# Kernel optimization log

Measured on AMD Instinct MI355X. Metric: run time of the kernel, lower is better.

The kernel has to match this reference:

```python
import jax, jax.numpy as jnp
import numpy as np

TGT_LEN, BS, SRC_LEN, VOCAB, DIM, EMB = 24, 16, 400, 32000, 256, 256


def setup_inputs() -> dict:
    key = jax.random.key(0)
    ks = jax.random.split(key, 16)
    g = lambda k, s, sc: jax.random.normal(k, s, dtype=jnp.float32) * sc
    return {
        "inputs": jax.random.randint(ks[0], (TGT_LEN, BS), 0, VOCAB),
        "src": jax.random.randint(ks[1], (SRC_LEN, BS), 0, VOCAB),
        "h_e": g(ks[2], (SRC_LEN, BS, DIM), 0.1),
        "h0": g(ks[3], (BS, DIM), 0.1),
        "c0": g(ks[4], (BS, DIM), 0.1),
        "W_emb": g(ks[5], (VOCAB, EMB), 0.05),
        "W_ih": g(ks[6], (4 * DIM, EMB), 0.05),
        "b_ih": g(ks[7], (4 * DIM,), 0.05),
        "W_hh": g(ks[8], (4 * DIM, DIM), 0.05),
        "b_hh": g(ks[9], (4 * DIM,), 0.05),
        "W_attn_enc": g(ks[10], (DIM, DIM), 0.05),
        "W_attn_dec": g(ks[11], (DIM, DIM), 0.05),
        "W_proj": g(ks[12], (EMB, 3 * DIM), 0.05),
        "W_u": g(ks[13], (1, 3 * DIM), 0.05),
        "b_u": g(ks[14], (1,), 0.05),
        "b_out": g(ks[15], (VOCAB, 1), 0.05),
        "pad_id": 1,
    }


def reference(inputs, src, h_e, h0, c0, W_emb, W_ih, b_ih, W_hh, b_hh,
              W_attn_enc, W_attn_dec, W_proj, W_u, b_u, b_out, pad_id):
    tgt_len, bs = inputs.shape
    vocab = W_emb.shape[0]
    dim = h0.shape[1]

    emb_seq = W_emb[inputs]                       # [T, bs, emb]
    # weight-shared output projection (sect 2.4), loop-invariant -> hoisted
    W_out = jnp.tanh(W_emb @ W_proj)              # [vocab, 3*dim]
    b_out_v = b_out[:, 0]                         # [vocab]
    w_u = W_u[0]                                  # [3*dim]
    src_ids = src.T                               # [bs, src_len]
    rows = jnp.arange(bs)[:, None]
    pos = jnp.arange(tgt_len)

    def lstm_cell(x, h, c):
        gates = x @ W_ih.T + b_ih + h @ W_hh.T + b_hh
        i, f, g_, o = jnp.split(gates, 4, axis=1)
        c_new = jax.nn.sigmoid(f) * c + jax.nn.sigmoid(i) * jnp.tanh(g_)
        h_new = jax.nn.sigmoid(o) * jnp.tanh(c_new)
        return h_new, c_new

    def step(carry, xs):
        h, c, E_hist, hd_hist = carry
        emb_t, t = xs
        h, c = lstm_cell(emb_t, h, c)
        hd_t = h                                   # [bs, dim]
        # --- temporal encoder intra-attention (eq. 3-5) ---
        q = hd_t @ W_attn_enc                      # [bs, dim]
        expE = jnp.exp(jnp.einsum('bd,sbd->bs', q, h_e))  # [bs, src]
        EE = jnp.where(t == 0, expE, expE / E_hist)
        E_hist = jnp.where(t == 0, expE, E_hist + expE)
        A_e = EE / EE.sum(axis=1, keepdims=True)
        c_e = jnp.einsum('bs,sbd->bd', A_e, h_e)
        # --- decoder intra-attention over hd_history (includes current step) ---
        hd_hist = hd_hist.at[t].set(hd_t)          # [T, bs, dim]
        qd = hd_t @ W_attn_dec
        Ed = jnp.einsum('bd,tbd->bt', qd, hd_hist)
        mask = pos[None, :] <= t
        EEd = jnp.where(mask, jnp.exp(Ed), 0.0)
        A_d = EEd / EEd.sum(axis=1, keepdims=True)
        cd = jnp.einsum('bt,tbd->bd', A_d, hd_hist)
        cd_t = jnp.where(t == 0, jnp.zeros_like(cd), cd)  # t==0: cd is zeros
        # --- pointer-generator (sect 2.3) ---
        feat = jnp.concatenate([hd_t, c_e, cd_t], axis=1)   # [bs, 3*dim]
        p_switch = jax.nn.sigmoid(feat @ w_u + b_u[0])       # [bs]
        logits = feat @ W_out.T + b_out_v                     # [bs, vocab]
        logits = logits.at[:, pad_id].set(-jnp.inf)
        p_gen = jax.nn.softmax(logits, axis=1)
        copy = jnp.zeros((bs, vocab), logits.dtype).at[rows, src_ids].add(A_e)
        scores_t = (copy + p_gen) * p_switch[:, None]
        return (h, c, E_hist, hd_hist), scores_t

    hd_hist0 = jnp.zeros((tgt_len, bs, dim), h0.dtype)
    E_hist0 = jnp.ones((bs, h_e.shape[0]), h0.dtype)
    _, scores = jax.lax.scan(step, (h0, c0, E_hist0, hd_hist0), (emb_seq, pos))
    return scores  # [T, bs, vocab] mixed copy/gen distribution per step
```

## Files before the change

kernel.cpp:

```cpp
#include <hip/hip_runtime.h>
#include <cstdint>
#include <cstddef>

#define TGT   24
#define BS    16
#define SRC   400
#define VOCABN 32000
#define DIM   256
#define NROW  (TGT*BS)
#define LSTM_NBLK 4

typedef __bf16 bf16_t;
typedef __bf16 v8bf __attribute__((ext_vector_type(8)));
typedef float  v4f  __attribute__((ext_vector_type(4)));
typedef unsigned int u32;
typedef unsigned short u16;

__device__ __forceinline__ float fast_tanh(float x) {
    float e = __expf(2.f*x);
    return 1.f - 2.f/(e + 1.f);
}

__global__ void k_prep(const float* __restrict__ Whh, const float* __restrict__ Wad,
                       const float* __restrict__ he,  const float* __restrict__ Wemb,
                       const float* __restrict__ Wproj, const float* __restrict__ Wae,
                       const float* __restrict__ Wih, const int* __restrict__ inputs,
                       const float* __restrict__ h0,
                       bf16_t* o_whh, bf16_t* o_wadT, bf16_t* o_he, bf16_t* o_heT,
                       bf16_t* o_wae, bf16_t* o_wih, bf16_t* o_wprojT, bf16_t* o_embA,
                       u32* o_hpk, u32* o_zero)
{
    const long S0=262144, S1=65536, S2=1638400, S3=1638400, S4=65536, S5=262144, S6=196608, S7=98304, S8=4096, S9=768;
    const long total = S0+S1+S2+S3+S4+S5+S6+S7+S8+S9;
    for (long i = (long)blockIdx.x*blockDim.x + threadIdx.x; i < total;
         i += (long)gridDim.x*blockDim.x) {
        long j = i;
        if (j < S0) { o_whh[j] = (bf16_t)Whh[j]; continue; }           j -= S0;
        if (j < S1) { long n = j>>8, k = j&255; o_wadT[j] = (bf16_t)Wad[k*DIM + n]; continue; } j -= S1;
        if (j < S2) { o_he[j] = (bf16_t)he[j]; continue; }             j -= S2;
        if (j < S3) {
            long b = j / 102400, rem = j % 102400, d = rem / 400, s = rem % 400;
            o_heT[j] = (bf16_t)he[(s*BS + b)*DIM + d]; continue; }     j -= S3;
        if (j < S4) { o_wae[j] = (bf16_t)Wae[j]; continue; }           j -= S4;
        if (j < S5) { o_wih[j] = (bf16_t)Wih[j]; continue; }           j -= S5;
        if (j < S6) { long n = j>>8, k = j&255; o_wprojT[j] = (bf16_t)Wproj[k*768 + n]; continue; } j -= S6;
        if (j < S7) { long r = j>>8, k = j&255; o_embA[j] = (bf16_t)Wemb[(long)inputs[r]*DIM + k]; continue; } j -= S7;
        if (j < S8) {
            float v = h0[j];
            bf16_t hi = (bf16_t)v;
            bf16_t lo = (bf16_t)(v - (float)hi);
            o_hpk[j] = (u32)(*(const u16*)&hi) | ((u32)(*(const u16*)&lo) << 16);
            continue; }                                                j -= S8;
        o_zero[j] = 0;
    }
}

__device__ __forceinline__ void gemm_tile(
    const int tid, bf16_t* As, bf16_t* Bs,
    const bf16_t* __restrict__ A, const float* __restrict__ A32,
    const bf16_t* __restrict__ B,
    const int tileIdx, const int N, const int K, const int Ntiles, const int mode,
    float* __restrict__ outF, bf16_t* __restrict__ outB,
    const float* __restrict__ bias0, const float* __restrict__ bias1)
{
    const int mt   = tileIdx / Ntiles, nt = tileIdx % Ntiles;
    const int m0   = mt*128, n0 = nt*128;
    const int lane = tid & 63, wave = tid >> 6;
    const int wm   = wave >> 1, wn = wave & 1;
    const int quad = lane >> 4, l16 = lane & 15;

    v4f acc[4][4];
#pragma unroll
    for (int i=0;i<4;i++)
#pragma unroll
        for (int j=0;j<4;j++) acc[i][j] = (v4f){0.f,0.f,0.f,0.f};

    const int srow = tid >> 1, shalf = tid & 1;
    const bf16_t* Ag   = A   ? A   + (size_t)(m0+srow)*K + shalf*16 : nullptr;
    const float*  Ag32 = A32 ? A32 + (size_t)(m0+srow)*K + shalf*16 : nullptr;
    const bf16_t* Bg = B + (size_t)(n0+srow)*K + shalf*16;
    bf16_t* AsW = &As[srow*40 + shalf*16];
    bf16_t* BsW = &Bs[srow*40 + shalf*16];

    for (int kc = 0; kc < K; kc += 32) {
        __syncthreads();
        uint4 b0 = *(const uint4*)(Bg + kc);
        uint4 b1 = *(const uint4*)(Bg + kc + 8);
        if (A32) {
            float4 f0 = *(const float4*)(Ag32 + kc);
            float4 f1 = *(const float4*)(Ag32 + kc + 4);
            float4 f2 = *(const float4*)(Ag32 + kc + 8);
            float4 f3 = *(const float4*)(Ag32 + kc + 12);
            v8bf u0, u1;
            u0[0]=(bf16_t)f0.x; u0[1]=(bf16_t)f0.y; u0[2]=(bf16_t)f0.z; u0[3]=(bf16_t)f0.w;
            u0[4]=(bf16_t)f1.x; u0[5]=(bf16_t)f1.y; u0[6]=(bf16_t)f1.z; u0[7]=(bf16_t)f1.w;
            u1[0]=(bf16_t)f2.x; u1[1]=(bf16_t)f2.y; u1[2]=(bf16_t)f2.z; u1[3]=(bf16_t)f2.w;
            u1[4]=(bf16_t)f3.x; u1[5]=(bf16_t)f3.y; u1[6]=(bf16_t)f3.z; u1[7]=(bf16_t)f3.w;
            *(v8bf*)AsW = u0; *(v8bf*)(AsW+8) = u1;
        } else {
            uint4 a0 = *(const uint4*)(Ag + kc);
            uint4 a1 = *(const uint4*)(Ag + kc + 8);
            *(uint4*)AsW = a0; *(uint4*)(AsW+8) = a1;
        }
        *(uint4*)BsW = b0; *(uint4*)(BsW+8) = b1;
        __syncthreads();
        v8bf af[4], bb[4];
#pragma unroll
        for (int i=0;i<4;i++) {
            af[i] = *(const v8bf*)&As[(wm*64 + i*16 + l16)*40 + quad*8];
            bb[i] = *(const v8bf*)&Bs[(wn*64 + i*16 + l16)*40 + quad*8];
        }
#pragma unroll
        for (int i=0;i<4;i++)
#pragma unroll
            for (int j=0;j<4;j++)
                acc[i][j] = __builtin_amdgcn_mfma_f32_16x16x32_bf16(af[i], bb[j], acc[i][j], 0,0,0);
    }

#pragma unroll
    for (int i=0;i<4;i++) {
#pragma unroll
        for (int j=0;j<4;j++) {
#pragma unroll
            for (int r=0;r<4;r++) {
                const int gr = m0 + wm*64 + i*16 + quad*4 + r;
                const int gc = n0 + wn*64 + j*16 + l16;
                const float v = acc[i][j][r];
                if (mode == 0)      outF[(size_t)gr*N + gc] = v + bias0[gc] + bias1[gc];
                else if (mode == 1) outB[(size_t)gr*N + gc] = (bf16_t)fast_tanh(v);
                else if (mode == 2) outB[(size_t)gr*N + gc] = (bf16_t)v;
                else if (mode == 4) outF[(size_t)gr*N + (gc & 255)*4 + (gc >> 8)] = v + bias0[gc] + bias1[gc];
            }
        }
    }
}

__global__ __launch_bounds__(256) void k_gemm2(
    const bf16_t* __restrict__ embA, const bf16_t* __restrict__ wih,
    float* __restrict__ xg, const float* __restrict__ b_ih, const float* __restrict__ b_hh,
    const bf16_t* __restrict__ heA, const bf16_t* __restrict__ waeB, bf16_t* __restrict__ keB)
{
    __shared__ bf16_t As[128*40];
    __shared__ bf16_t Bs[128*40];
    if (blockIdx.x < 24)
        gemm_tile(threadIdx.x, As, Bs, embA, nullptr, wih, blockIdx.x, 1024, 256, 8, 4,
                  xg, nullptr, b_ih, b_hh);
    else
        gemm_tile(threadIdx.x, As, Bs, heA, nullptr, waeB, blockIdx.x - 24, 256, 256, 2, 2,
                  nullptr, keB, nullptr, nullptr);
}

__global__ __launch_bounds__(256) void k_gemm3(
    const bf16_t* __restrict__ A, const bf16_t* __restrict__ B,
    float* __restrict__ outF, const float* __restrict__ bias0,
    const int* __restrict__ padp, float* __restrict__ rsum)
{
    __shared__ bf16_t As[128*72];
    __shared__ bf16_t Bs[128*72];
    const int tid = threadIdx.x;
    const int mt = blockIdx.x / 250, nt = blockIdx.x % 250;
    const int m0 = mt*128, n0 = nt*128;
    const int lane = tid & 63, wave = tid >> 6;
    const int wm = wave >> 1, wn = wave & 1;
    const int quad = lane >> 4, l16 = lane & 15;

    v4f acc[4][4];
#pragma unroll
    for (int i=0;i<4;i++)
#pragma unroll
        for (int j=0;j<4;j++) acc[i][j] = (v4f){0.f,0.f,0.f,0.f};

    const int srow = tid >> 1, shalf = tid & 1;
    const bf16_t* Ag = A + (size_t)(m0+srow)*768 + shalf*32;
    const bf16_t* Bg = B + (size_t)(n0+srow)*768 + shalf*32;
    bf16_t* AsW = &As[srow*72 + shalf*32];
    bf16_t* BsW = &Bs[srow*72 + shalf*32];

    for (int kc = 0; kc < 768; kc += 64) {
        __syncthreads();
        uint4 a0 = *(const uint4*)(Ag + kc);
        uint4 a1 = *(const uint4*)(Ag + kc + 8);
        uint4 a2 = *(const uint4*)(Ag + kc + 16);
        uint4 a3 = *(const uint4*)(Ag + kc + 24);
        uint4 b0 = *(const uint4*)(Bg + kc);
        uint4 b1 = *(const uint4*)(Bg + kc + 8);
        uint4 b2 = *(const uint4*)(Bg + kc + 16);
        uint4 b3 = *(const uint4*)(Bg + kc + 24);
        *(uint4*)(AsW)    = a0; *(uint4*)(AsW+8)  = a1;
        *(uint4*)(AsW+16) = a2; *(uint4*)(AsW+24) = a3;
        *(uint4*)(BsW)    = b0; *(uint4*)(BsW+8)  = b1;
        *(uint4*)(BsW+16) = b2; *(uint4*)(BsW+24) = b3;
        __syncthreads();
#pragma unroll
        for (int kk = 0; kk < 2; ++kk) {
            v8bf af[4], bb[4];
#pragma unroll
            for (int i=0;i<4;i++) {
                af[i] = *(const v8bf*)&As[(wm*64 + i*16 + l16)*72 + kk*32 + quad*8];
                bb[i] = *(const v8bf*)&Bs[(wn*64 + i*16 + l16)*72 + kk*32 + quad*8];
            }
#pragma unroll
            for (int i=0;i<4;i++)
#pragma unroll
                for (int j=0;j<4;j++)
                    acc[i][j] = __builtin_amdgcn_mfma_f32_16x16x32_bf16(af[i], bb[j], acc[i][j], 0,0,0);
        }
    }

    const int pad = *padp;
    float* rs = (float*)As;
    __syncthreads();
    if (tid < 128) rs[tid] = 0.f;
    __syncthreads();
#pragma unroll
    for (int i=0;i<4;i++) {
        float rloc[4] = {0.f,0.f,0.f,0.f};
#pragma unroll
        for (int j=0;j<4;j++) {
#pragma unroll
            for (int r=0;r<4;r++) {
                const int gr = m0 + wm*64 + i*16 + quad*4 + r;
                const int gc = n0 + wn*64 + j*16 + l16;
                const float ex = (gc == pad) ? 0.f : __expf(acc[i][j][r] + bias0[gc]);
                outF[(size_t)gr*VOCABN + gc] = ex;
                rloc[r] += ex;
            }
        }
#pragma unroll
        for (int r=0;r<4;r++)
            atomicAdd(&rs[wm*64 + i*16 + quad*4 + r], rloc[r]);
    }
    __syncthreads();
    if (tid < 128) atomicAdd(&rsum[m0 + tid], rs[tid]);
}

__device__ __forceinline__ void gridbar(int* bar, int target) {
    __syncthreads();
    if (threadIdx.x == 0) {
        __threadfence();
        __hip_atomic_fetch_add(bar, 1, __ATOMIC_ACQ_REL, __HIP_MEMORY_SCOPE_AGENT);
        while (__hip_atomic_load(bar, __ATOMIC_ACQUIRE, __HIP_MEMORY_SCOPE_AGENT) < target) { }
        __threadfence();
    }
    __syncthreads();
}

__global__ __launch_bounds__(512, 2) void k_lstm(
    const bf16_t* __restrict__ Whh, const float* __restrict__ xgT,
    const float* __restrict__ c0,
    u32* __restrict__ hpk,
    float* __restrict__ hallF,
    int* __restrict__ bar)
{
    __shared__ float gl[16][260];

    const int tid = threadIdx.x;
    const int k = blockIdx.x;
    const int w = tid >> 6, lane = tid & 63;
    const int l16 = lane & 15, quad = lane >> 4;

    v8bf wb[2][8];
#pragma unroll
    for (int ct = 0; ct < 2; ++ct) {
        const int c = w*32 + ct*16 + l16;
        const int row = (c >> 6)*256 + k*64 + (c & 63);
#pragma unroll
        for (int kc = 0; kc < 8; ++kc)
            wb[ct][kc] = *(const v8bf*)&Whh[(size_t)row*DIM + kc*32 + quad*8];
    }

    float cst[2];
#pragma unroll
    for (int e = 0; e < 2; ++e) {
        const int li = tid + e*512;
        cst[e] = c0[(li >> 6)*DIM + k*64 + (li & 63)];
    }

    for (int step = 0; step < TGT; ++step) {
        uint4 pq[8][2];
#pragma unroll
        for (int kc = 0; kc < 8; ++kc) {
            const uint4* pp = (const uint4*)&hpk[l16*DIM + kc*32 + quad*8];
            pq[kc][0] = pp[0]; pq[kc][1] = pp[1];
        }
        float4 xv[2];
#pragma unroll
        for (int e = 0; e < 2; ++e) {
            const int li = tid + e*512;
            const int b = li >> 6, dd = li & 63;
            xv[e] = *(const float4*)&xgT[((size_t)(step*BS + b)*DIM + k*64 + dd)*4];
        }
        v8bf ahi[8], alo[8];
#pragma unroll
        for (int kc = 0; kc < 8; ++kc) {
            const u32 uu[8] = {pq[kc][0].x, pq[kc][0].y, pq[kc][0].z, pq[kc][0].w,
                               pq[kc][1].x, pq[kc][1].y, pq[kc][1].z, pq[kc][1].w};
#pragma unroll
            for (int j = 0; j < 8; ++j) {
                union { u32 u; u16 s[2]; } x; x.u = uu[j];
                ahi[kc][j] = *(const bf16_t*)&x.s[0];
                alo[kc][j] = *(const bf16_t*)&x.s[1];
            }
        }

        v4f acc[2] = {(v4f){0.f,0.f,0.f,0.f}, (v4f){0.f,0.f,0.f,0.f}};
#pragma unroll
        for (int kc = 0; kc < 8; ++kc)
#pragma unroll
            for (int ct = 0; ct < 2; ++ct) {
                acc[ct] = __builtin_amdgcn_mfma_f32_16x16x32_bf16(ahi[kc], wb[ct][kc], acc[ct], 0,0,0);
                acc[ct] = __builtin_amdgcn_mfma_f32_16x16x32_bf16(alo[kc], wb[ct][kc], acc[ct], 0,0,0);
            }
#pragma unroll
        for (int ct = 0; ct < 2; ++ct) {
            const int c = w*32 + ct*16 + l16;
#pragma unroll
            for (int r = 0; r < 4; ++r)
                gl[quad*4 + r][c] = acc[ct][r];
        }
        __syncthreads();
        float hnv[2];
#pragma unroll
        for (int e = 0; e < 2; ++e) {
            const int li = tid + e*512;
            const int b = li >> 6, dd = li & 63;
            const int d = k*64 + dd;
            const float gi = gl[b][dd]        + xv[e].x;
            const float gf = gl[b][64 + dd]   + xv[e].y;
            const float gg = gl[b][128 + dd]  + xv[e].z;
            const float go = gl[b][192 + dd]  + xv[e].w;
            const float si = 1.f/(1.f+__expf(-gi));
            const float sf = 1.f/(1.f+__expf(-gf));
            const float so = 1.f/(1.f+__expf(-go));
            const float cn = sf*cst[e] + si*fast_tanh(gg);
            const float hn = so*fast_tanh(cn);
            cst[e] = cn;
            hnv[e] = hn;
            const bf16_t hi = (bf16_t)hn;
            const bf16_t lo = (bf16_t)(hn - (float)hi);
            const u32 pk = (u32)(*(const u16*)&hi) | ((u32)(*(const u16*)&lo) << 16);
            __hip_atomic_store(&hpk[b*DIM + d], pk, __ATOMIC_RELAXED, __HIP_MEMORY_SCOPE_AGENT);
        }
        if (step < TGT-1) gridbar(bar, (step+1)*LSTM_NBLK);
#pragma unroll
        for (int e = 0; e < 2; ++e) {
            const int li = tid + e*512;
            const int b = li >> 6, dd = li & 63;
            const int d = k*64 + dd;
            union { float f; u32 u; } cv; cv.f = hnv[e];
            __hip_atomic_store((u32*)&hallF[(size_t)(step*BS + b)*DIM + d], cv.u,
                               __ATOMIC_RELAXED, __HIP_MEMORY_SCOPE_AGENT);
        }
    }
}

__device__ __forceinline__ void escore_body(const int blk, const int tid, float* hS,
    const bf16_t* __restrict__ ke, const float* __restrict__ hallF, float* __restrict__ expE)
{
    const int t = blk >> 4, b = blk & 15;
    hS[tid] = hallF[(size_t)(t*BS + b)*DIM + tid];
    __syncthreads();
    for (int s = tid; s < SRC; s += 256) {
        const v8bf* kp = (const v8bf*)(ke + ((size_t)s*BS + b)*DIM);
        float e = 0.f;
#pragma unroll 8
        for (int m=0;m<32;m++) {
            v8bf kv = kp[m];
#pragma unroll
            for (int i=0;i<8;i++) e += (float)kv[i]*hS[m*8+i];
        }
        expE[((size_t)t*BS + b)*SRC + s] = __expf(e);
    }
}

__global__ __launch_bounds__(256) void k_esq(
    const bf16_t* __restrict__ ke, const float* __restrict__ hallF, float* __restrict__ expE,
    const bf16_t* __restrict__ wadT, bf16_t* __restrict__ qdG)
{
    __shared__ __align__(16) char shb[20480];
    if (blockIdx.x < NROW) {
        escore_body(blockIdx.x, threadIdx.x, (float*)shb, ke, hallF, expE);
        return;
    }
    gemm_tile(threadIdx.x, (bf16_t*)shb, (bf16_t*)(shb + 10240), nullptr, hallF, wadT,
              blockIdx.x - NROW, 256, 256, 2, 2, nullptr, qdG, nullptr, nullptr);
}

__global__ __launch_bounds__(256) void k_prefix(float* __restrict__ expE)
{
    const int i = blockIdx.x*256 + threadIdx.x;
    if (i >= BS*SRC) return;
    const int b = i / SRC, s = i % SRC;
    float c = 0.f;
    for (int t = 0; t < TGT; ++t) {
        const size_t idx = ((size_t)t*BS + b)*SRC + s;
        c += expE[idx];
        expE[idx] = c;
    }
}

__device__ void attn_body(char* sh, const int blk, const int tid,
    const float* __restrict__ cumE, const bf16_t* __restrict__ heT,
    const float* __restrict__ hallF, const bf16_t* __restrict__ qdG,
    const float* __restrict__ wu, const float* __restrict__ bu,
    bf16_t* __restrict__ feat, float* __restrict__ Ae, float* __restrict__ ps)
{
    float* hS   = (float*)sh;
    float* qdS  = hS + 256;
    float* eeS  = qdS + 256;
    float* adS  = eeS + 400;
    float* red  = adS + 24;
    float* misc = red + 4;
    const int t = blk >> 4, b = blk & 15;

    hS[tid]  = hallF[(size_t)(t*BS + b)*DIM + tid];
    qdS[tid] = (float)qdG[(size_t)(t*BS + b)*DIM + tid];
    __syncthreads();

    for (int s = tid; s < SRC; s += 256) {
        if (t == 0) {
            eeS[s] = cumE[(size_t)b*SRC + s];
        } else {
            const float prev = cumE[((size_t)(t-1)*BS + b)*SRC + s];
            const float cur  = cumE[((size_t)t*BS + b)*SRC + s];
            eeS[s] = (cur - prev) / prev;
        }
    }
    __syncthreads();
    {
        float pa = 0.f;
        for (int s = tid; s < SRC; s += 256) pa += eeS[s];
#pragma unroll
        for (int o=32;o>0;o>>=1) pa += __shfl_down(pa, o);
        if ((tid & 63) == 0) red[tid>>6] = pa;
        __syncthreads();
        if (tid == 0) misc[0] = 1.f/(red[0]+red[1]+red[2]+red[3]);
        __syncthreads();
    }
    const float inv_es = misc[0];
    for (int s = tid; s < SRC; s += 256)
        Ae[((size_t)t*BS + b)*SRC + s] = eeS[s] * inv_es;

    float ce;
    {
        const v8bf* hp = (const v8bf*)(heT + ((size_t)b*DIM + tid)*SRC);
        float acc = 0.f;
#pragma unroll 10
        for (int m=0;m<50;m++) {
            v8bf hv = hp[m];
#pragma unroll
            for (int i=0;i<8;i++) acc += (float)hv[i]*eeS[m*8+i];
        }
        ce = acc * inv_es;
    }

    {
        const int wv = tid >> 6, ln = tid & 63;
        for (int tau = wv; tau <= t; tau += 4) {
            float4 a = *(const float4*)(hallF + ((size_t)(tau*BS + b))*DIM + ln*4);
            float e = a.x*qdS[ln*4] + a.y*qdS[ln*4+1] + a.z*qdS[ln*4+2] + a.w*qdS[ln*4+3];
#pragma unroll
            for (int o=32;o>0;o>>=1) e += __shfl_down(e, o);
            if (ln == 0) adS[tau] = __expf(e);
        }
    }
    __syncthreads();
    if (tid < 64) {
        float v = (tid <= t) ? adS[tid] : 0.f;
#pragma unroll
        for (int o=32;o>0;o>>=1) v += __shfl_down(v, o);
        if (tid == 0) misc[1] = 1.f/v;
    }
    __syncthreads();
    float cd = 0.f;
    for (int tau = 0; tau <= t; ++tau)
        cd += adS[tau] * hallF[((size_t)(tau*BS + b))*DIM + tid];
    cd *= misc[1];
    if (t == 0) cd = 0.f;

    const float hd = hS[tid];
    const size_t fr = ((size_t)t*BS + b)*768;
    feat[fr + tid]       = (bf16_t)hd;
    feat[fr + 256 + tid] = (bf16_t)ce;
    feat[fr + 512 + tid] = (bf16_t)cd;
    float pw = hd*wu[tid] + ce*wu[256 + tid] + cd*wu[512 + tid];
#pragma unroll
    for (int o=32;o>0;o>>=1) pw += __shfl_down(pw, o);
    if ((tid & 63) == 0) red[tid>>6] = pw;
    __syncthreads();
    if (tid == 0) {
        float s = red[0]+red[1]+red[2]+red[3];
        ps[t*BS + b] = 1.f/(1.f+__expf(-(s + bu[0])));
    }
}

__global__ __launch_bounds__(256) void k_attnw(
    const float* __restrict__ cumE, const bf16_t* __restrict__ heT,
    const float* __restrict__ hallF, const bf16_t* __restrict__ qdG,
    const float* __restrict__ wu, const float* __restrict__ bu,
    bf16_t* __restrict__ feat, float* __restrict__ Ae, float* __restrict__ ps,
    const float* __restrict__ Wemb, const bf16_t* __restrict__ wprojT,
    bf16_t* __restrict__ woutB)
{
    __shared__ __align__(16) char shb[20480];
    if (blockIdx.x < NROW) {
        attn_body(shb, blockIdx.x, threadIdx.x, cumE, heT, hallF, qdG, wu, bu, feat, Ae, ps);
        return;
    }
    gemm_tile(threadIdx.x, (bf16_t*)shb, (bf16_t*)(shb + 10240), nullptr, Wemb, wprojT,
              blockIdx.x - NROW, 768, 256, 6, 1,
              nullptr, woutB, nullptr, nullptr);
}

__global__ __launch_bounds__(256) void k_final(
    float* __restrict__ out, const float* __restrict__ rsum,
    const float* __restrict__ ps, const int* __restrict__ src,
    const float* __restrict__ Ae)
{
    const int r = blockIdx.x;
    const int b = r & (BS-1);
    const float p  = ps[r];
    const float sc = p / rsum[r];
    float4* o4 = (float4*)(out + (size_t)r*VOCABN);
    for (int i = threadIdx.x; i < VOCABN/4; i += 256) {
        float4 v = o4[i];
        v.x*=sc; v.y*=sc; v.z*=sc; v.w*=sc;
        o4[i] = v;
    }
    __syncthreads();
    for (int s = threadIdx.x; s < SRC; s += 256) {
        const int v = src[s*BS + b];
        atomicAdd(&out[(size_t)r*VOCABN + v], Ae[(size_t)r*SRC + s] * p);
    }
}

#define O_WHH    0u
#define O_WADT   524288u
#define O_HEBF   655360u
#define O_HET    3932160u
#define O_KE     7208960u
#define O_WAE    10485760u
#define O_WPROJT 10616832u
#define O_WIH    11010048u
#define O_EMBA   11534336u
#define O_WOUT   11730944u
#define O_XG     60882944u
#define O_HALLF  62455808u
#define O_QD     63045632u
#define O_EXPE   63242240u
#define O_FEAT   63856640u
#define O_AE     64446464u
#define O_PS     65060864u
#define O_BAR    65062400u
#define O_RSUM   65063936u

extern "C" void kernel_launch(void* const* d_in, const int* in_sizes, int n_in,
                              void* d_out, int out_size, void* d_ws, size_t ws_size,
                              hipStream_t stream)
{
    const int*   inputs = (const int*)  d_in[0];
    const int*   src    = (const int*)  d_in[1];
    const float* h_e    = (const float*)d_in[2];
    const float* h0     = (const float*)d_in[3];
    const float* c0     = (const float*)d_in[4];
    const float* W_emb  = (const float*)d_in[5];
    const float* W_ih   = (const float*)d_in[6];
    const float* b_ih   = (const float*)d_in[7];
    const float* W_hh   = (const float*)d_in[8];
    const float* b_hh   = (const float*)d_in[9];
    const float* W_ae   = (const float*)d_in[10];
    const float* W_ad   = (const float*)d_in[11];
    const float* W_proj = (const float*)d_in[12];
    const float* W_u    = (const float*)d_in[13];
    const float* b_u    = (const float*)d_in[14];
    const float* b_out  = (const float*)d_in[15];
    const int*   pad_id = (const int*)  d_in[16];

    char* w = (char*)d_ws;
    bf16_t* whh_bf  = (bf16_t*)(w + O_WHH);
    bf16_t* wadT_bf = (bf16_t*)(w + O_WADT);
    bf16_t* he_bf   = (bf16_t*)(w + O_HEBF);
    bf16_t* heT_bf  = (bf16_t*)(w + O_HET);
    bf16_t* ke_bf   = (bf16_t*)(w + O_KE);
    bf16_t* wae_bf  = (bf16_t*)(w + O_WAE);
    bf16_t* wprojT  = (bf16_t*)(w + O_WPROJT);
    bf16_t* wih_bf  = (bf16_t*)(w + O_WIH);
    bf16_t* embA_bf = (bf16_t*)(w + O_EMBA);
    bf16_t* wout_bf = (bf16_t*)(w + O_WOUT);
    float*  xg      = (float*) (w + O_XG);
    float*  hallF   = (float*) (w + O_HALLF);
    bf16_t* qdG     = (bf16_t*)(w + O_QD);
    float*  expE    = (float*) (w + O_EXPE);
    u32*    hpk     = (u32*)   (w + O_EXPE);
    bf16_t* feat_bf = (bf16_t*)(w + O_FEAT);
    float*  Ae      = (float*) (w + O_AE);
    float*  ps      = (float*) (w + O_PS);
    int*    bar     = (int*)   (w + O_BAR);
    u32*    zeroreg = (u32*)   (w + O_BAR);
    float*  rsum    = (float*) (w + O_RSUM);
    float*  out     = (float*)d_out;

    k_prep<<<1024, 256, 0, stream>>>(W_hh, W_ad, h_e, W_emb, W_proj, W_ae, W_ih, inputs, h0,
                                     whh_bf, wadT_bf, he_bf, heT_bf,
                                     wae_bf, wih_bf, wprojT, embA_bf, hpk, zeroreg);
    k_gemm2<<<124, 256, 0, stream>>>(embA_bf, wih_bf, xg, b_ih, b_hh,
                                     he_bf, wae_bf, ke_bf);
    k_lstm<<<LSTM_NBLK, 512, 0, stream>>>(whh_bf, xg, c0, hpk, hallF, bar);
    k_esq<<<NROW + 6, 256, 0, stream>>>(ke_bf, hallF, expE, wadT_bf, qdG);
    k_prefix<<<25, 256, 0, stream>>>(expE);
    k_attnw<<<NROW + 1500, 256, 0, stream>>>(expE, heT_bf, hallF, qdG, W_u, b_u,
                                             feat_bf, Ae, ps,
                                             W_emb, wprojT, wout_bf);
    k_gemm3<<<750, 256, 0, stream>>>(feat_bf, wout_bf, out, b_out, pad_id, rsum);
    k_final<<<NROW, 256, 0, stream>>>(out, rsum, ps, src, Ae);
}
```

Measured before the change: 439.8 us.

## Drop h_e transpose copy and move weight transposes into gemm2 via LDS tiles

```diff
diff --git a/kernel.cpp b/kernel.cpp
--- a/kernel.cpp
+++ b/kernel.cpp
@@ -21,38 +21,59 @@
     return 1.f - 2.f/(e + 1.f);
 }
 
-__global__ void k_prep(const float* __restrict__ Whh, const float* __restrict__ Wad,
-                       const float* __restrict__ he,  const float* __restrict__ Wemb,
-                       const float* __restrict__ Wproj, const float* __restrict__ Wae,
+__global__ void k_prep(const float* __restrict__ Whh, const float* __restrict__ he,
+                       const float* __restrict__ Wemb, const float* __restrict__ Wae,
                        const float* __restrict__ Wih, const int* __restrict__ inputs,
                        const float* __restrict__ h0,
-                       bf16_t* o_whh, bf16_t* o_wadT, bf16_t* o_he, bf16_t* o_heT,
-                       bf16_t* o_wae, bf16_t* o_wih, bf16_t* o_wprojT, bf16_t* o_embA,
-                       u32* o_hpk, u32* o_zero)
-{
-    const long S0=262144, S1=65536, S2=1638400, S3=1638400, S4=65536, S5=262144, S6=196608, S7=98304, S8=4096, S9=768;
-    const long total = S0+S1+S2+S3+S4+S5+S6+S7+S8+S9;
+                       bf16_t* o_whh, bf16_t* o_he, bf16_t* o_wae, bf16_t* o_wih,
+                       bf16_t* o_embA, u32* o_hpk, u32* o_zero)
+{
+    const long S0=262144, S1=1638400, S2=65536, S3=262144, S4=98304, S5=4096, S6=768;
+    const long total = S0+S1+S2+S3+S4+S5+S6;
     for (long i = (long)blockIdx.x*blockDim.x + threadIdx.x; i < total;
          i += (long)gridDim.x*blockDim.x) {
         long j = i;
         if (j < S0) { o_whh[j] = (bf16_t)Whh[j]; continue; }           j -= S0;
-        if (j < S1) { long n = j>>8, k = j&255; o_wadT[j] = (bf16_t)Wad[k*DIM + n]; continue; } j -= S1;
-        if (j < S2) { o_he[j] = (bf16_t)he[j]; continue; }             j -= S2;
-        if (j < S3) {
-            long b = j / 102400, rem = j % 102400, d = rem / 400, s = rem % 400;
-            o_heT[j] = (bf16_t)he[(s*BS + b)*DIM + d]; continue; }     j -= S3;
-        if (j < S4) { o_wae[j] = (bf16_t)Wae[j]; continue; }           j -= S4;
-        if (j < S5) { o_wih[j] = (bf16_t)Wih[j]; continue; }           j -= S5;
-        if (j < S6) { long n = j>>8, k = j&255; o_wprojT[j] = (bf16_t)Wproj[k*768 + n]; continue; } j -= S6;
-        if (j < S7) { long r = j>>8, k = j&255; o_embA[j] = (bf16_t)Wemb[(long)inputs[r]*DIM + k]; continue; } j -= S7;
-        if (j < S8) {
+        if (j < S1) { o_he[j] = (bf16_t)he[j]; continue; }             j -= S1;
+        if (j < S2) { o_wae[j] = (bf16_t)Wae[j]; continue; }           j -= S2;
+        if (j < S3) { o_wih[j] = (bf16_t)Wih[j]; continue; }           j -= S3;
+        if (j < S4) { long r = j>>8, k = j&255; o_embA[j] = (bf16_t)Wemb[(long)inputs[r]*DIM + k]; continue; } j -= S4;
+        if (j < S5) {
             float v = h0[j];
             bf16_t hi = (bf16_t)v;
             bf16_t lo = (bf16_t)(v - (float)hi);
             o_hpk[j] = (u32)(*(const u16*)&hi) | ((u32)(*(const u16*)&lo) << 16);
-            continue; }                                                j -= S8;
+            continue; }                                                j -= S5;
         o_zero[j] = 0;
     }
+}
+
+__device__ void transpose_tile(const int tid, float* lds ,
+                               const float* __restrict__ in, bf16_t* __restrict__ out,
+                               const int R, const int C, const int tileIdx)
+{
+    const int tilesC = C >> 6;
+    const int tr = (tileIdx / tilesC) << 6;
+    const int tc = (tileIdx % tilesC) << 6;
+    const int r0 = tid >> 4;
+    const int c0 = (tid & 15) * 4;
+#pragma unroll
+    for (int p = 0; p < 4; ++p) {
+        const int r = p*16 + r0;
+        float4 v = *(const float4*)&in[(size_t)(tr + r)*C + tc + c0];
+        lds[r*65 + c0+0] = v.x; lds[r*65 + c0+1] = v.y;
+        lds[r*65 + c0+2] = v.z; lds[r*65 + c0+3] = v.w;
+    }
+    __syncthreads();
+    const int oc  = tid >> 2;
+    const int orr = (tid & 3) * 16;
+    bf16_t tmp[16];
+#pragma unroll
+    for (int k = 0; k < 16; ++k)
+        tmp[k] = (bf16_t)lds[(orr + k)*65 + oc];
+    bf16_t* op = &out[(size_t)(tc + oc)*R + tr + orr];
+    *(uint4*)op       = ((uint4*)tmp)[0];
+    *(uint4*)(op + 8) = ((uint4*)tmp)[1];
 }
 
 __device__ __forceinline__ void gemm_tile(
@@ -138,16 +159,25 @@
 __global__ __launch_bounds__(256) void k_gemm2(
     const bf16_t* __restrict__ embA, const bf16_t* __restrict__ wih,
     float* __restrict__ xg, const float* __restrict__ b_ih, const float* __restrict__ b_hh,
-    const bf16_t* __restrict__ heA, const bf16_t* __restrict__ waeB, bf16_t* __restrict__ keB)
-{
-    __shared__ bf16_t As[128*40];
-    __shared__ bf16_t Bs[128*40];
-    if (blockIdx.x < 24)
-        gemm_tile(threadIdx.x, As, Bs, embA, nullptr, wih, blockIdx.x, 1024, 256, 8, 4,
-                  xg, nullptr, b_ih, b_hh);
-    else
-        gemm_tile(threadIdx.x, As, Bs, heA, nullptr, waeB, blockIdx.x - 24, 256, 256, 2, 2,
-                  nullptr, keB, nullptr, nullptr);
+    const bf16_t* __restrict__ heA, const bf16_t* __restrict__ waeB, bf16_t* __restrict__ keB,
+    const float* __restrict__ Wproj, bf16_t* __restrict__ wprojT,
+    const float* __restrict__ Wad, bf16_t* __restrict__ wadT)
+{
+    __shared__ __align__(16) char shb[20480];
+    const int bid = blockIdx.x;
+    if (bid < 24) {
+        gemm_tile(threadIdx.x, (bf16_t*)shb, (bf16_t*)(shb + 10240), embA, nullptr, wih,
+                  bid, 1024, 256, 8, 4, xg, nullptr, b_ih, b_hh);
+        return;
+    }
+    if (bid < 124) {
+        gemm_tile(threadIdx.x, (bf16_t*)shb, (bf16_t*)(shb + 10240), heA, nullptr, waeB,
+                  bid - 24, 256, 256, 2, 2, nullptr, keB, nullptr, nullptr);
+        return;
+    }
+    float* tl = (float*)shb;
+    if (bid < 172) { transpose_tile(threadIdx.x, tl, Wproj, wprojT, 256, 768, bid - 124); return; }
+    transpose_tile(threadIdx.x, tl, Wad, wadT, 256, 256, bid - 172);
 }
 
 __global__ __launch_bounds__(256) void k_gemm3(
@@ -400,7 +430,7 @@
 }
 
 __device__ void attn_body(char* sh, const int blk, const int tid,
-    const float* __restrict__ cumE, const bf16_t* __restrict__ heT,
+    const float* __restrict__ cumE, const bf16_t* __restrict__ heA,
     const float* __restrict__ hallF, const bf16_t* __restrict__ qdG,
     const float* __restrict__ wu, const float* __restrict__ bu,
     bf16_t* __restrict__ feat, float* __restrict__ Ae, float* __restrict__ ps)
@@ -443,15 +473,15 @@
 
     float ce;
     {
-        const v8bf* hp = (const v8bf*)(heT + ((size_t)b*DIM + tid)*SRC);
-        float acc = 0.f;
-#pragma unroll 10
-        for (int m=0;m<50;m++) {
-            v8bf hv = hp[m];
-#pragma unroll
-            for (int i=0;i<8;i++) acc += (float)hv[i]*eeS[m*8+i];
-        }
-        ce = acc * inv_es;
+        const bf16_t* hp = heA + (size_t)b*DIM + tid;
+        float a0=0.f, a1=0.f, a2=0.f, a3=0.f;
+        for (int s = 0; s < SRC; s += 4) {
+            a0 += (float)hp[(size_t)(s+0)*BS*DIM] * eeS[s+0];
+            a1 += (float)hp[(size_t)(s+1)*BS*DIM] * eeS[s+1];
+            a2 += (float)hp[(size_t)(s+2)*BS*DIM] * eeS[s+2];
+            a3 += (float)hp[(size_t)(s+3)*BS*DIM] * eeS[s+3];
+        }
+        ce = ((a0+a1)+(a2+a3)) * inv_es;
     }
 
     {
@@ -495,7 +525,7 @@
 }
 
 __global__ __launch_bounds__(256) void k_attnw(
-    const float* __restrict__ cumE, const bf16_t* __restrict__ heT,
+    const float* __restrict__ cumE, const bf16_t* __restrict__ heA,
     const float* __restrict__ hallF, const bf16_t* __restrict__ qdG,
     const float* __restrict__ wu, const float* __restrict__ bu,
     bf16_t* __restrict__ feat, float* __restrict__ Ae, float* __restrict__ ps,
@@ -504,7 +534,7 @@
 {
     __shared__ __align__(16) char shb[20480];
     if (blockIdx.x < NROW) {
-        attn_body(shb, blockIdx.x, threadIdx.x, cumE, heT, hallF, qdG, wu, bu, feat, Ae, ps);
+        attn_body(shb, blockIdx.x, threadIdx.x, cumE, heA, hallF, qdG, wu, bu, feat, Ae, ps);
         return;
     }
     gemm_tile(threadIdx.x, (bf16_t*)shb, (bf16_t*)(shb + 10240), nullptr, Wemb, wprojT,
@@ -537,7 +567,6 @@
 #define O_WHH    0u
 #define O_WADT   524288u
 #define O_HEBF   655360u
-#define O_HET    3932160u
 #define O_KE     7208960u
 #define O_WAE    10485760u
 #define O_WPROJT 10616832u
@@ -580,7 +609,6 @@
     bf16_t* whh_bf  = (bf16_t*)(w + O_WHH);
     bf16_t* wadT_bf = (bf16_t*)(w + O_WADT);
     bf16_t* he_bf   = (bf16_t*)(w + O_HEBF);
-    bf16_t* heT_bf  = (bf16_t*)(w + O_HET);
     bf16_t* ke_bf   = (bf16_t*)(w + O_KE);
     bf16_t* wae_bf  = (bf16_t*)(w + O_WAE);
     bf16_t* wprojT  = (bf16_t*)(w + O_WPROJT);
@@ -600,15 +628,16 @@
     float*  rsum    = (float*) (w + O_RSUM);
     float*  out     = (float*)d_out;
 
-    k_prep<<<1024, 256, 0, stream>>>(W_hh, W_ad, h_e, W_emb, W_proj, W_ae, W_ih, inputs, h0,
-                                     whh_bf, wadT_bf, he_bf, heT_bf,
-                                     wae_bf, wih_bf, wprojT, embA_bf, hpk, zeroreg);
-    k_gemm2<<<124, 256, 0, stream>>>(embA_bf, wih_bf, xg, b_ih, b_hh,
-                                     he_bf, wae_bf, ke_bf);
+    k_prep<<<1024, 256, 0, stream>>>(W_hh, h_e, W_emb, W_ae, W_ih, inputs, h0,
+                                     whh_bf, he_bf, wae_bf, wih_bf,
+                                     embA_bf, hpk, zeroreg);
+    k_gemm2<<<188, 256, 0, stream>>>(embA_bf, wih_bf, xg, b_ih, b_hh,
+                                     he_bf, wae_bf, ke_bf,
+                                     W_proj, wprojT, W_ad, wadT_bf);
     k_lstm<<<LSTM_NBLK, 512, 0, stream>>>(whh_bf, xg, c0, hpk, hallF, bar);
     k_esq<<<NROW + 6, 256, 0, stream>>>(ke_bf, hallF, expE, wadT_bf, qdG);
     k_prefix<<<25, 256, 0, stream>>>(expE);
-    k_attnw<<<NROW + 1500, 256, 0, stream>>>(expE, heT_bf, hallF, qdG, W_u, b_u,
+    k_attnw<<<NROW + 1500, 256, 0, stream>>>(expE, he_bf, hallF, qdG, W_u, b_u,
                                              feat_bf, Ae, ps,
                                              W_emb, wprojT, wout_bf);
     k_gemm3<<<750, 256, 0, stream>>>(feat_bf, wout_bf, out, b_out, pad_id, rsum);
```

New measurement: 414.3 us. 5.8% less time.
